# Optimization experiments

Hardware: AMD Instinct MI355X
Metric: run time of the kernel (lower is better)

The kernel has to match this reference:

```python
import jax, jax.numpy as jnp
import numpy as np

B, E, N, D, H = 4, 8, 1024, 1024, 4096


def setup_inputs() -> dict:
    key = jax.random.key(0)
    k1, k2, k3 = jax.random.split(key, 3)
    x = jax.random.normal(k1, (B, E, N, D), dtype=jnp.float32)
    # expert MLP weights: Linear(D,H) -> GELU -> Linear(H,D), per expert
    w1 = jax.random.normal(k2, (E, D, H), dtype=jnp.float32) * 0.02
    b1 = jnp.zeros((E, H), dtype=jnp.float32)
    w2 = jax.random.normal(k3, (E, H, D), dtype=jnp.float32) * 0.02
    b2 = jnp.zeros((E, D), dtype=jnp.float32)
    return {"x": x, "w1": w1, "b1": b1, "w2": w2, "b2": b2}


def reference(x, w1, b1, w2, b2):
    # x: [b, e, n, d]. Original rearranges to 'e b n d' and applies expert i
    # to slice i; a batched einsum over the expert axis is the same math.
    h = jnp.einsum('bend,edh->benh', x, w1) + b1[:, None, :]  # [b,e,n,H]
    h = jax.nn.gelu(h, approximate=False)  # torch nn.GELU default = exact erf
    out = jnp.einsum('benh,ehd->bend', h, w2) + b2[:, None, :]  # [b,e,n,d]
    return out
```

## Files before the change

### kernel.cpp

```cpp
#include <hip/hip_runtime.h>
#include <stdint.h>


typedef __attribute__((ext_vector_type(8))) short short8;
typedef __attribute__((ext_vector_type(4))) float f32x4;

__device__ __forceinline__ unsigned short f2b(float f){
  union { float f; unsigned int u; } v; v.f = f;
  unsigned int r = v.u + 0x7fffu + ((v.u >> 16) & 1u);
  return (unsigned short)(r >> 16);
}

__device__ __forceinline__ float gelu_fast(float v){
  float v2 = v * v;
  float w = v * (-2.302217529693f + -0.102943795894f * v2);
  float e = __builtin_amdgcn_exp2f(w);
  return v * __builtin_amdgcn_rcpf(1.0f + e);
}

__device__ __forceinline__ void glds16(const void* g, const void* l){
  __builtin_amdgcn_global_load_lds((const __attribute__((address_space(1))) uint32_t*)g,
                                   (__attribute__((address_space(3))) uint32_t*)l, 16, 0, 0);
}

#define BAR() do{ asm volatile("" ::: "memory"); __builtin_amdgcn_s_barrier(); asm volatile("" ::: "memory"); }while(0)


__global__ void cvt_x_kernel(const float* __restrict__ src, unsigned short* __restrict__ dst, int n4){
  int i = blockIdx.x * blockDim.x + threadIdx.x;
  int stride = gridDim.x * blockDim.x;
  for (; i < n4; i += stride){
    float4 v = ((const float4*)src)[i];
    ushort4 o;
    o.x = f2b(v.x); o.y = f2b(v.y); o.z = f2b(v.z); o.w = f2b(v.w);
    ((ushort4*)dst)[i] = o;
  }
}

__global__ void transpose_cvt(const float* __restrict__ src, unsigned short* __restrict__ dst, int R, int C){
  __shared__ float t[64][65];
  const int e = blockIdx.z;
  src += (size_t)e * R * C;
  dst += (size_t)e * R * C;
  const int r0 = blockIdx.y * 64, c0 = blockIdx.x * 64;
  const int tid = threadIdx.x;
  const int lr = tid >> 4;
  const int lc4 = (tid & 15) * 4;
  #pragma unroll
  for (int p2 = 0; p2 < 4; p2++){
    int r = lr + p2 * 16;
    float4 v = *(const float4*)(src + (size_t)(r0 + r) * C + (c0 + lc4));
    t[r][lc4+0] = v.x; t[r][lc4+1] = v.y; t[r][lc4+2] = v.z; t[r][lc4+3] = v.w;
  }
  __syncthreads();
  #pragma unroll
  for (int p2 = 0; p2 < 4; p2++){
    int c = lr + p2 * 16;
    ushort4 o;
    o.x = f2b(t[lc4+0][c]); o.y = f2b(t[lc4+1][c]);
    o.z = f2b(t[lc4+2][c]); o.w = f2b(t[lc4+3][c]);
    *(ushort4*)(dst + (size_t)(c0 + c) * R + (r0 + lc4)) = o;
  }
}


template<int PHASE1>
__global__ __launch_bounds__(512, 2) void gemm256(
    const unsigned short* __restrict__ A,
    const unsigned short* __restrict__ Bt,
    const float* __restrict__ bias,
    void* __restrict__ Out,
    int p0)
{
  constexpr int M  = 1024;
  constexpr int K  = PHASE1 ? 1024 : 4096;
  constexpr int Nd = PHASE1 ? 4096 : 1024;
  constexpr int TM = M / 256, TN = Nd / 256;
  constexpr int NT = K / 64;

  const int cpx = gridDim.x >> 3;
  const int bid = (blockIdx.x & 7) * cpx + (blockIdx.x >> 3);
  const int tn = bid % TN;
  const int t2 = bid / TN;
  const int tm = t2 % TM;
  const int cp = t2 / TM;
  const int p  = p0 + cp, e = p & 7;
  const int m0 = tm * 256, n0 = tn * 256;

  const unsigned short* Ag = A  + (size_t)(PHASE1 ? p : cp) * M * K + (size_t)m0 * K;
  const unsigned short* Bg = Bt + (size_t)e * Nd * K + (size_t)n0 * K;
  const float*          bp = bias + (size_t)e * Nd;

  __shared__ __align__(16) unsigned short lds[65536];

  const int tid = threadIdx.x;
  const int w = tid >> 6, lane = tid & 63;
  const int wr = w >> 2, wc = w & 3;
  const int c15 = lane & 15, q = lane >> 4;

  const int trow = (w << 3) + (lane >> 3);
  const int scol = ((lane & 7) ^ (trow & 7)) << 3;
  const unsigned short* pA0 = Ag + (size_t)(trow       ) * K + scol;
  const unsigned short* pA1 = Ag + (size_t)(trow +  64) * K + scol;
  const unsigned short* pA2 = Ag + (size_t)(trow + 128) * K + scol;
  const unsigned short* pA3 = Ag + (size_t)(trow + 192) * K + scol;
  const unsigned short* pB0 = Bg + (size_t)(trow       ) * K + scol;
  const unsigned short* pB1 = Bg + (size_t)(trow +  64) * K + scol;
  const unsigned short* pB2 = Bg + (size_t)(trow + 128) * K + scol;
  const unsigned short* pB3 = Bg + (size_t)(trow + 192) * K + scol;
  const int wof = w << 9;

  const int rA64 = (wr * 128 + c15) << 6;
  const int rB64 = (wc * 64  + c15) << 6;
  const int cx0 = ( q      ^ (c15 & 7)) << 3;
  const int cx1 = ((q ^ 4) ^ (c15 & 7)) << 3;

  float bv[4];
  #pragma unroll
  for (int nf = 0; nf < 4; ++nf) bv[nf] = bp[n0 + wc * 64 + nf * 16 + c15];

  f32x4 acc[8][4];
  #pragma unroll
  for (int i = 0; i < 8; i++)
    #pragma unroll
    for (int j = 0; j < 4; j++) acc[i][j] = (f32x4)(bv[j]);

  glds16(pA0, lds + wof);
  glds16(pA1, lds + wof + 4096);
  glds16(pA2, lds + wof + 8192);
  glds16(pA3, lds + wof + 12288);
  glds16(pB0, lds + wof + 32768);
  glds16(pB1, lds + wof + 32768 + 4096);
  glds16(pB2, lds + wof + 32768 + 8192);
  glds16(pB3, lds + wof + 32768 + 12288);
  glds16(pA0 + 64, lds + wof + 16384);
  glds16(pA1 + 64, lds + wof + 16384 + 4096);
  asm volatile("s_waitcnt vmcnt(2)" ::: "memory");
  BAR();

  short8 af[4][2], bf0[2][2], bf1[2][2];

#define TILE_BODY(CB, PF1, PF2, VM) do{                                         \
    constexpr int AB  = (CB) * 16384;                                           \
    constexpr int BB  = 32768 + (CB) * 16384;                                   \
    constexpr int ABn = ((CB) ^ 1) * 16384;                                     \
    constexpr int BBn = 32768 + (((CB) ^ 1) * 16384);                           \
    constexpr int O1  = (CB) ? 128 : 64;                                        \
    constexpr int O2  = (CB) ? 192 : 128;                                       \
       \
    _Pragma("unroll")                                                           \
    for (int mf = 0; mf < 4; ++mf){                                             \
      af[mf][0] = *(const short8*)(lds + AB + rA64 + mf * 1024 + cx0);          \
      af[mf][1] = *(const short8*)(lds + AB + rA64 + mf * 1024 + cx1);          \
    }                                                                           \
    _Pragma("unroll")                                                           \
    for (int nf = 0; nf < 2; ++nf){                                             \
      bf0[nf][0] = *(const short8*)(lds + BB + rB64 + nf * 1024 + cx0);         \
      bf0[nf][1] = *(const short8*)(lds + BB + rB64 + nf * 1024 + cx1);         \
    }                                                                           \
    if (PF1){ glds16(pA2 + O1, lds + ABn + 8192 + wof);                         \
              glds16(pA3 + O1, lds + ABn + 12288 + wof); }                      \
    BAR();                                                                      \
    __builtin_amdgcn_s_setprio(1);                                              \
    _Pragma("unroll")                                                           \
    for (int mf = 0; mf < 4; ++mf)                                              \
      _Pragma("unroll")                                                         \
      for (int nf = 0; nf < 2; ++nf){                                           \
        acc[mf][nf] = __builtin_amdgcn_mfma_f32_16x16x32_bf16(af[mf][0], bf0[nf][0], acc[mf][nf], 0, 0, 0); \
        acc[mf][nf] = __builtin_amdgcn_mfma_f32_16x16x32_bf16(af[mf][1], bf0[nf][1], acc[mf][nf], 0, 0, 0); \
      }                                                                         \
    __builtin_amdgcn_s_setprio(0);                                              \
    BAR();                                                                      \
                      \
    _Pragma("unroll")                                                           \
    for (int nf = 0; nf < 2; ++nf){                                             \
      bf1[nf][0] = *(const short8*)(lds + BB + rB64 + 2048 + nf * 1024 + cx0);  \
      bf1[nf][1] = *(const short8*)(lds + BB + rB64 + 2048 + nf * 1024 + cx1);  \
    }                                                                           \
    if (PF1){ glds16(pB0 + O1, lds + BBn + wof);                                \
              glds16(pB1 + O1, lds + BBn + 4096 + wof); }                       \
    BAR();                                                                      \
    __builtin_amdgcn_s_setprio(1);                                              \
    _Pragma("unroll")                                                           \
    for (int mf = 0; mf < 4; ++mf)                                              \
      _Pragma("unroll")                                                         \
      for (int nf = 0; nf < 2; ++nf){                                           \
        acc[mf][2+nf] = __builtin_amdgcn_mfma_f32_16x16x32_bf16(af[mf][0], bf1[nf][0], acc[mf][2+nf], 0, 0, 0); \
        acc[mf][2+nf] = __builtin_amdgcn_mfma_f32_16x16x32_bf16(af[mf][1], bf1[nf][1], acc[mf][2+nf], 0, 0, 0); \
      }                                                                         \
    __builtin_amdgcn_s_setprio(0);                                              \
    BAR();                                                                      \
                    \
    _Pragma("unroll")                                                           \
    for (int mf = 0; mf < 4; ++mf){                                             \
      af[mf][0] = *(const short8*)(lds + AB + rA64 + 4096 + mf * 1024 + cx0);   \
      af[mf][1] = *(const short8*)(lds + AB + rA64 + 4096 + mf * 1024 + cx1);   \
    }                                                                           \
    if (PF1){ glds16(pB2 + O1, lds + BBn + 8192 + wof);                         \
              glds16(pB3 + O1, lds + BBn + 12288 + wof); }                      \
    BAR();                                                                      \
    __builtin_amdgcn_s_setprio(1);                                              \
    _Pragma("unroll")                                                           \
    for (int mf = 0; mf < 4; ++mf)                                              \
      _Pragma("unroll")                                                         \
      for (int nf = 0; nf < 2; ++nf){                                           \
        acc[4+mf][2+nf] = __builtin_amdgcn_mfma_f32_16x16x32_bf16(af[mf][0], bf1[nf][0], acc[4+mf][2+nf], 0, 0, 0); \
        acc[4+mf][2+nf] = __builtin_amdgcn_mfma_f32_16x16x32_bf16(af[mf][1], bf1[nf][1], acc[4+mf][2+nf], 0, 0, 0); \
      }                                                                         \
    __builtin_amdgcn_s_setprio(0);                                              \
    BAR();                                                                      \
          \
    if (PF2){ glds16(pA0 + O2, lds + AB + wof);                                 \
              glds16(pA1 + O2, lds + AB + 4096 + wof); }                        \
    BAR();                                                                      \
    __builtin_amdgcn_s_setprio(1);                                              \
    _Pragma("unroll")                                                           \
    for (int mf = 0; mf < 4; ++mf)                                              \
      _Pragma("unroll")                                                         \
      for (int nf = 0; nf < 2; ++nf){                                           \
        acc[4+mf][nf] = __builtin_amdgcn_mfma_f32_16x16x32_bf16(af[mf][0], bf0[nf][0], acc[4+mf][nf], 0, 0, 0); \
        acc[4+mf][nf] = __builtin_amdgcn_mfma_f32_16x16x32_bf16(af[mf][1], bf0[nf][1], acc[4+mf][nf], 0, 0, 0); \
      }                                                                         \
    __builtin_amdgcn_s_setprio(0);                                              \
    if ((VM) >= 0){                                                             \
      if ((VM) == 2) asm volatile("s_waitcnt vmcnt(2)" ::: "memory");           \
      else           asm volatile("s_waitcnt vmcnt(0)" ::: "memory");           \
    }                                                                           \
    BAR();                                                                      \
  }while(0)

  for (int kt2 = 0; kt2 + 2 < NT; kt2 += 2){
    TILE_BODY(0, 1, 1, 2);
    TILE_BODY(1, 1, 1, 2);
    pA0 += 128; pA1 += 128; pA2 += 128; pA3 += 128;
    pB0 += 128; pB1 += 128; pB2 += 128; pB3 += 128;
  }
  TILE_BODY(0, 1, 0, 0);
  TILE_BODY(1, 0, 0, -1);
#undef TILE_BODY

  #pragma unroll
  for (int mf = 0; mf < 8; ++mf){
    const int row = m0 + wr * 128 + mf * 16 + q * 4;
    #pragma unroll
    for (int nf = 0; nf < 4; ++nf){
      const int col = n0 + wc * 64 + nf * 16 + c15;
      #pragma unroll
      for (int r = 0; r < 4; ++r){
        float v = acc[mf][nf][r];
        if constexpr (PHASE1){
          ((unsigned short*)Out)[(size_t)cp * M * Nd + (size_t)(row + r) * Nd + col] = f2b(gelu_fast(v));
        } else {
          ((float*)Out)[(size_t)p * M * Nd + (size_t)(row + r) * Nd + col] = v;
        }
      }
    }
  }
}


extern "C" void kernel_launch(void* const* d_in, const int* in_sizes, int n_in,
                              void* d_out, int out_size, void* d_ws, size_t ws_size,
                              hipStream_t stream){
  const float* x  = (const float*)d_in[0];
  const float* w1 = (const float*)d_in[1];
  const float* b1 = (const float*)d_in[2];
  const float* w2 = (const float*)d_in[3];
  const float* b2 = (const float*)d_in[4];
  float* out = (float*)d_out;

  unsigned short* xb  = (unsigned short*)d_ws;
  unsigned short* w1t = (unsigned short*)((char*)d_ws + ((size_t)64  << 20));
  unsigned short* w2t = (unsigned short*)((char*)d_ws + ((size_t)128 << 20));
  unsigned short* hb  = (unsigned short*)((char*)d_ws + ((size_t)192 << 20));

  size_t avail = ws_size > ((size_t)192 << 20) ? ws_size - ((size_t)192 << 20) : 0;
  int ppc = (int)(avail / ((size_t)8 << 20));
  if (ppc > 32) ppc = 32;
  if (ppc < 1) return;

  cvt_x_kernel<<<2048, 256, 0, stream>>>(x, xb, 8 * 1024 * 1024);
  transpose_cvt<<<dim3(64, 16, 8), 256, 0, stream>>>(w1, w1t, 1024, 4096);
  transpose_cvt<<<dim3(16, 64, 8), 256, 0, stream>>>(w2, w2t, 4096, 1024);

  for (int p0 = 0; p0 < 32; p0 += ppc){
    int np = (32 - p0 < ppc) ? (32 - p0) : ppc;
    gemm256<1><<<dim3(np * 4 * 16), 512, 0, stream>>>(xb, w1t, b1, hb, p0);
    gemm256<0><<<dim3(np * 4 * 4),  512, 0, stream>>>(hb, w2t, b2, out, p0);
  }
}
```

Before: 624.6 us.

## Restructure GEMM main loop to prefetch LDS fragments across phases with fewer barriers

Reworks the bf16 MFMA tile body so that A/B fragments for the next phase and next k-tile are read from LDS before the barrier that ends the current phase, cutting the number of barriers per tile from eight to four. It also reorders which global-to-LDS prefetches are issued in each phase (A rows 1 and 3 early, all four B slices together, A rows 0 and 2 late). The goal is to overlap LDS reads with MFMA work and reduce synchronization stalls. In exchange it holds more fragment registers live and depends on subtle ordering between LDS writes and reads across buffers, which could cause races or register pressure.

```diff
diff --git a/kernel.cpp b/kernel.cpp
--- a/kernel.cpp
+++ b/kernel.cpp
@@ -125,6 +125,26 @@
     #pragma unroll
     for (int j = 0; j < 4; j++) acc[i][j] = (f32x4)(bv[j]);
 
+  short8 afA[2][2], afB[2][2], bf0_[2][2], bf1_[2][2];
+
+#define LD(OFS) (*(const short8*)(lds + (OFS)))
+#define RD_AFA(BASE) do{ _Pragma("unroll") for (int mi=0;mi<2;++mi){ \
+    afA[mi][0] = LD((BASE) + rA64 + mi*1024 + cx0); \
+    afA[mi][1] = LD((BASE) + rA64 + mi*1024 + cx1); } }while(0)
+#define RD_AFB(BASE) do{ _Pragma("unroll") for (int mi=0;mi<2;++mi){ \
+    afB[mi][0] = LD((BASE) + rA64 + 2048 + mi*1024 + cx0); \
+    afB[mi][1] = LD((BASE) + rA64 + 2048 + mi*1024 + cx1); } }while(0)
+#define RD_BF0(BASE) do{ _Pragma("unroll") for (int nf=0;nf<2;++nf){ \
+    bf0_[nf][0] = LD((BASE) + rB64 + nf*1024 + cx0); \
+    bf0_[nf][1] = LD((BASE) + rB64 + nf*1024 + cx1); } }while(0)
+#define RD_BF1(BASE) do{ _Pragma("unroll") for (int nf=0;nf<2;++nf){ \
+    bf1_[nf][0] = LD((BASE) + rB64 + 2048 + nf*1024 + cx0); \
+    bf1_[nf][1] = LD((BASE) + rB64 + 2048 + nf*1024 + cx1); } }while(0)
+#define Q8(MO,NO,AF,BF) do{ _Pragma("unroll") for (int mi=0;mi<2;++mi) \
+    _Pragma("unroll") for (int nf=0;nf<2;++nf){ \
+      acc[(MO)+mi][(NO)+nf] = __builtin_amdgcn_mfma_f32_16x16x32_bf16(AF[mi][0], BF[nf][0], acc[(MO)+mi][(NO)+nf],0,0,0); \
+      acc[(MO)+mi][(NO)+nf] = __builtin_amdgcn_mfma_f32_16x16x32_bf16(AF[mi][1], BF[nf][1], acc[(MO)+mi][(NO)+nf],0,0,0); } }while(0)
+
   glds16(pA0, lds + wof);
   glds16(pA1, lds + wof + 4096);
   glds16(pA2, lds + wof + 8192);
@@ -134,110 +154,63 @@
   glds16(pB2, lds + wof + 32768 + 8192);
   glds16(pB3, lds + wof + 32768 + 12288);
   glds16(pA0 + 64, lds + wof + 16384);
-  glds16(pA1 + 64, lds + wof + 16384 + 4096);
+  glds16(pA2 + 64, lds + wof + 16384 + 8192);
   asm volatile("s_waitcnt vmcnt(2)" ::: "memory");
   BAR();
-
-  short8 af[4][2], bf0[2][2], bf1[2][2];
-
-#define TILE_BODY(CB, PF1, PF2, VM) do{                                         \
+  RD_AFA(0); RD_AFB(0); RD_BF0(32768);
+
+#define TILE_P(CB, PF1, PF2) do{                                                \
     constexpr int AB  = (CB) * 16384;                                           \
     constexpr int BB  = 32768 + (CB) * 16384;                                   \
     constexpr int ABn = ((CB) ^ 1) * 16384;                                     \
     constexpr int BBn = 32768 + (((CB) ^ 1) * 16384);                           \
     constexpr int O1  = (CB) ? 128 : 64;                                        \
     constexpr int O2  = (CB) ? 192 : 128;                                       \
-       \
-    _Pragma("unroll")                                                           \
-    for (int mf = 0; mf < 4; ++mf){                                             \
-      af[mf][0] = *(const short8*)(lds + AB + rA64 + mf * 1024 + cx0);          \
-      af[mf][1] = *(const short8*)(lds + AB + rA64 + mf * 1024 + cx1);          \
-    }                                                                           \
-    _Pragma("unroll")                                                           \
-    for (int nf = 0; nf < 2; ++nf){                                             \
-      bf0[nf][0] = *(const short8*)(lds + BB + rB64 + nf * 1024 + cx0);         \
-      bf0[nf][1] = *(const short8*)(lds + BB + rB64 + nf * 1024 + cx1);         \
-    }                                                                           \
-    if (PF1){ glds16(pA2 + O1, lds + ABn + 8192 + wof);                         \
+                        \
+    RD_BF1(BB);                                                                 \
+    if (PF1){ glds16(pA1 + O1, lds + ABn + 4096 + wof);                         \
               glds16(pA3 + O1, lds + ABn + 12288 + wof); }                      \
-    BAR();                                                                      \
-    __builtin_amdgcn_s_setprio(1);                                              \
-    _Pragma("unroll")                                                           \
-    for (int mf = 0; mf < 4; ++mf)                                              \
-      _Pragma("unroll")                                                         \
-      for (int nf = 0; nf < 2; ++nf){                                           \
-        acc[mf][nf] = __builtin_amdgcn_mfma_f32_16x16x32_bf16(af[mf][0], bf0[nf][0], acc[mf][nf], 0, 0, 0); \
-        acc[mf][nf] = __builtin_amdgcn_mfma_f32_16x16x32_bf16(af[mf][1], bf0[nf][1], acc[mf][nf], 0, 0, 0); \
-      }                                                                         \
-    __builtin_amdgcn_s_setprio(0);                                              \
-    BAR();                                                                      \
-                      \
-    _Pragma("unroll")                                                           \
-    for (int nf = 0; nf < 2; ++nf){                                             \
-      bf1[nf][0] = *(const short8*)(lds + BB + rB64 + 2048 + nf * 1024 + cx0);  \
-      bf1[nf][1] = *(const short8*)(lds + BB + rB64 + 2048 + nf * 1024 + cx1);  \
-    }                                                                           \
+    __builtin_amdgcn_s_setprio(1);                                              \
+    Q8(0,0,afA,bf0_); Q8(2,0,afB,bf0_);                                         \
+    __builtin_amdgcn_s_setprio(0);                                              \
+    BAR();                                                                      \
+        \
     if (PF1){ glds16(pB0 + O1, lds + BBn + wof);                                \
-              glds16(pB1 + O1, lds + BBn + 4096 + wof); }                       \
-    BAR();                                                                      \
-    __builtin_amdgcn_s_setprio(1);                                              \
-    _Pragma("unroll")                                                           \
-    for (int mf = 0; mf < 4; ++mf)                                              \
-      _Pragma("unroll")                                                         \
-      for (int nf = 0; nf < 2; ++nf){                                           \
-        acc[mf][2+nf] = __builtin_amdgcn_mfma_f32_16x16x32_bf16(af[mf][0], bf1[nf][0], acc[mf][2+nf], 0, 0, 0); \
-        acc[mf][2+nf] = __builtin_amdgcn_mfma_f32_16x16x32_bf16(af[mf][1], bf1[nf][1], acc[mf][2+nf], 0, 0, 0); \
-      }                                                                         \
-    __builtin_amdgcn_s_setprio(0);                                              \
-    BAR();                                                                      \
-                    \
-    _Pragma("unroll")                                                           \
-    for (int mf = 0; mf < 4; ++mf){                                             \
-      af[mf][0] = *(const short8*)(lds + AB + rA64 + 4096 + mf * 1024 + cx0);   \
-      af[mf][1] = *(const short8*)(lds + AB + rA64 + 4096 + mf * 1024 + cx1);   \
-    }                                                                           \
-    if (PF1){ glds16(pB2 + O1, lds + BBn + 8192 + wof);                         \
+              glds16(pB1 + O1, lds + BBn + 4096 + wof);                         \
+              glds16(pB2 + O1, lds + BBn + 8192 + wof);                         \
               glds16(pB3 + O1, lds + BBn + 12288 + wof); }                      \
-    BAR();                                                                      \
-    __builtin_amdgcn_s_setprio(1);                                              \
-    _Pragma("unroll")                                                           \
-    for (int mf = 0; mf < 4; ++mf)                                              \
-      _Pragma("unroll")                                                         \
-      for (int nf = 0; nf < 2; ++nf){                                           \
-        acc[4+mf][2+nf] = __builtin_amdgcn_mfma_f32_16x16x32_bf16(af[mf][0], bf1[nf][0], acc[4+mf][2+nf], 0, 0, 0); \
-        acc[4+mf][2+nf] = __builtin_amdgcn_mfma_f32_16x16x32_bf16(af[mf][1], bf1[nf][1], acc[4+mf][2+nf], 0, 0, 0); \
-      }                                                                         \
-    __builtin_amdgcn_s_setprio(0);                                              \
-    BAR();                                                                      \
-          \
+    __builtin_amdgcn_s_setprio(1);                                              \
+    Q8(0,2,afA,bf1_); Q8(2,2,afB,bf1_);                                         \
+    __builtin_amdgcn_s_setprio(0);                                              \
+    RD_AFA(AB + 4096);                                                          \
+    BAR();                                                                      \
+    \
+    RD_AFB(AB + 4096);                                                          \
     if (PF2){ glds16(pA0 + O2, lds + AB + wof);                                 \
-              glds16(pA1 + O2, lds + AB + 4096 + wof); }                        \
-    BAR();                                                                      \
-    __builtin_amdgcn_s_setprio(1);                                              \
-    _Pragma("unroll")                                                           \
-    for (int mf = 0; mf < 4; ++mf)                                              \
-      _Pragma("unroll")                                                         \
-      for (int nf = 0; nf < 2; ++nf){                                           \
-        acc[4+mf][nf] = __builtin_amdgcn_mfma_f32_16x16x32_bf16(af[mf][0], bf0[nf][0], acc[4+mf][nf], 0, 0, 0); \
-        acc[4+mf][nf] = __builtin_amdgcn_mfma_f32_16x16x32_bf16(af[mf][1], bf0[nf][1], acc[4+mf][nf], 0, 0, 0); \
-      }                                                                         \
-    __builtin_amdgcn_s_setprio(0);                                              \
-    if ((VM) >= 0){                                                             \
-      if ((VM) == 2) asm volatile("s_waitcnt vmcnt(2)" ::: "memory");           \
-      else           asm volatile("s_waitcnt vmcnt(0)" ::: "memory");           \
-    }                                                                           \
+              glds16(pA2 + O2, lds + AB + 8192 + wof); }                        \
+    __builtin_amdgcn_s_setprio(1);                                              \
+    Q8(4,2,afA,bf1_); Q8(6,2,afB,bf1_);                                         \
+    __builtin_amdgcn_s_setprio(0);                                              \
+    if (PF1){ if (PF2){ asm volatile("s_waitcnt vmcnt(2)" ::: "memory"); }      \
+              else    { asm volatile("s_waitcnt vmcnt(0)" ::: "memory"); } }    \
+    BAR();                                                                      \
+                \
+    __builtin_amdgcn_s_setprio(1);                                              \
+    Q8(4,0,afA,bf0_); Q8(6,0,afB,bf0_);                                         \
+    __builtin_amdgcn_s_setprio(0);                                              \
+    if (PF1){ RD_AFA(ABn); RD_AFB(ABn); RD_BF0(BBn); }                          \
     BAR();                                                                      \
   }while(0)
 
-  for (int kt2 = 0; kt2 + 2 < NT; kt2 += 2){
-    TILE_BODY(0, 1, 1, 2);
-    TILE_BODY(1, 1, 1, 2);
+  for (int kt2 = 0; kt2 < NT - 2; kt2 += 2){
+    TILE_P(0, 1, 1);
+    TILE_P(1, 1, 1);
     pA0 += 128; pA1 += 128; pA2 += 128; pA3 += 128;
     pB0 += 128; pB1 += 128; pB2 += 128; pB3 += 128;
   }
-  TILE_BODY(0, 1, 0, 0);
-  TILE_BODY(1, 0, 0, -1);
-#undef TILE_BODY
+  TILE_P(0, 1, 0);
+  TILE_P(1, 0, 0);
+#undef TILE_P
 
   #pragma unroll
   for (int mf = 0; mf < 8; ++mf){
```

Result: slower. 780.9 us (+25.0%).

## Reorder prefetch issue and split waitcnts to load A rows just in time

Applied to the files above, without the earlier changes.

Changes the order of the global-to-LDS prefetches inside the double-buffered GEMM tile loop. B is now prefetched first, and the A sub-tiles are grouped so the half that the next tile reads first arrives earliest. A second, finer vmcnt wait is added mid-tile, letting more loads stay in flight while only the data needed next must have landed. This aims to hide more global latency behind MFMA work, at the cost of depending on correct ordering and vmcnt accounting.

```diff
diff --git a/kernel.cpp b/kernel.cpp
--- a/kernel.cpp
+++ b/kernel.cpp
@@ -24,6 +24,10 @@
 }
 
 #define BAR() do{ asm volatile("" ::: "memory"); __builtin_amdgcn_s_barrier(); asm volatile("" ::: "memory"); }while(0)
+#define VMW(N) do{ if ((N)==6) asm volatile("s_waitcnt vmcnt(6)":::"memory"); \
+  else if ((N)==4) asm volatile("s_waitcnt vmcnt(4)":::"memory"); \
+  else if ((N)==2) asm volatile("s_waitcnt vmcnt(2)":::"memory"); \
+  else if ((N)==0) asm volatile("s_waitcnt vmcnt(0)":::"memory"); }while(0)
 
 
 __global__ void cvt_x_kernel(const float* __restrict__ src, unsigned short* __restrict__ dst, int n4){
@@ -134,20 +138,20 @@
   glds16(pB2, lds + wof + 32768 + 8192);
   glds16(pB3, lds + wof + 32768 + 12288);
   glds16(pA0 + 64, lds + wof + 16384);
-  glds16(pA1 + 64, lds + wof + 16384 + 4096);
+  glds16(pA2 + 64, lds + wof + 16384 + 8192);
   asm volatile("s_waitcnt vmcnt(2)" ::: "memory");
   BAR();
 
   short8 af[4][2], bf0[2][2], bf1[2][2];
 
-#define TILE_BODY(CB, PF1, PF2, VM) do{                                         \
+#define TILE_BODY(CB, SB1, SA2, W1, W3) do{                                     \
     constexpr int AB  = (CB) * 16384;                                           \
     constexpr int BB  = 32768 + (CB) * 16384;                                   \
     constexpr int ABn = ((CB) ^ 1) * 16384;                                     \
     constexpr int BBn = 32768 + (((CB) ^ 1) * 16384);                           \
     constexpr int O1  = (CB) ? 128 : 64;                                        \
     constexpr int O2  = (CB) ? 192 : 128;                                       \
-       \
+              \
     _Pragma("unroll")                                                           \
     for (int mf = 0; mf < 4; ++mf){                                             \
       af[mf][0] = *(const short8*)(lds + AB + rA64 + mf * 1024 + cx0);          \
@@ -158,8 +162,8 @@
       bf0[nf][0] = *(const short8*)(lds + BB + rB64 + nf * 1024 + cx0);         \
       bf0[nf][1] = *(const short8*)(lds + BB + rB64 + nf * 1024 + cx1);         \
     }                                                                           \
-    if (PF1){ glds16(pA2 + O1, lds + ABn + 8192 + wof);                         \
-              glds16(pA3 + O1, lds + ABn + 12288 + wof); }                      \
+    if (SB1){ glds16(pB0 + O1, lds + BBn + wof);                                \
+              glds16(pB1 + O1, lds + BBn + 4096 + wof); }                       \
     BAR();                                                                      \
     __builtin_amdgcn_s_setprio(1);                                              \
     _Pragma("unroll")                                                           \
@@ -171,14 +175,14 @@
       }                                                                         \
     __builtin_amdgcn_s_setprio(0);                                              \
     BAR();                                                                      \
-                      \
+                  \
     _Pragma("unroll")                                                           \
     for (int nf = 0; nf < 2; ++nf){                                             \
       bf1[nf][0] = *(const short8*)(lds + BB + rB64 + 2048 + nf * 1024 + cx0);  \
       bf1[nf][1] = *(const short8*)(lds + BB + rB64 + 2048 + nf * 1024 + cx1);  \
     }                                                                           \
-    if (PF1){ glds16(pB0 + O1, lds + BBn + wof);                                \
-              glds16(pB1 + O1, lds + BBn + 4096 + wof); }                       \
+    if (SB1){ glds16(pB2 + O1, lds + BBn + 8192 + wof);                         \
+              glds16(pB3 + O1, lds + BBn + 12288 + wof); }                      \
     BAR();                                                                      \
     __builtin_amdgcn_s_setprio(1);                                              \
     _Pragma("unroll")                                                           \
@@ -189,15 +193,16 @@
         acc[mf][2+nf] = __builtin_amdgcn_mfma_f32_16x16x32_bf16(af[mf][1], bf1[nf][1], acc[mf][2+nf], 0, 0, 0); \
       }                                                                         \
     __builtin_amdgcn_s_setprio(0);                                              \
-    BAR();                                                                      \
-                    \
+    if ((W1) >= 0) VMW(W1);                                                     \
+    BAR();                                                                      \
+                           \
     _Pragma("unroll")                                                           \
     for (int mf = 0; mf < 4; ++mf){                                             \
       af[mf][0] = *(const short8*)(lds + AB + rA64 + 4096 + mf * 1024 + cx0);   \
       af[mf][1] = *(const short8*)(lds + AB + rA64 + 4096 + mf * 1024 + cx1);   \
     }                                                                           \
-    if (PF1){ glds16(pB2 + O1, lds + BBn + 8192 + wof);                         \
-              glds16(pB3 + O1, lds + BBn + 12288 + wof); }                      \
+    if (SB1){ glds16(pA1 + O1, lds + ABn + 4096 + wof);                         \
+              glds16(pA3 + O1, lds + ABn + 12288 + wof); }                      \
     BAR();                                                                      \
     __builtin_amdgcn_s_setprio(1);                                              \
     _Pragma("unroll")                                                           \
@@ -210,8 +215,8 @@
     __builtin_amdgcn_s_setprio(0);                                              \
     BAR();                                                                      \
           \
-    if (PF2){ glds16(pA0 + O2, lds + AB + wof);                                 \
-              glds16(pA1 + O2, lds + AB + 4096 + wof); }                        \
+    if (SA2){ glds16(pA0 + O2, lds + AB + wof);                                 \
+              glds16(pA2 + O2, lds + AB + 8192 + wof); }                        \
     BAR();                                                                      \
     __builtin_amdgcn_s_setprio(1);                                              \
     _Pragma("unroll")                                                           \
@@ -222,21 +227,18 @@
         acc[4+mf][nf] = __builtin_amdgcn_mfma_f32_16x16x32_bf16(af[mf][1], bf0[nf][1], acc[4+mf][nf], 0, 0, 0); \
       }                                                                         \
     __builtin_amdgcn_s_setprio(0);                                              \
-    if ((VM) >= 0){                                                             \
-      if ((VM) == 2) asm volatile("s_waitcnt vmcnt(2)" ::: "memory");           \
-      else           asm volatile("s_waitcnt vmcnt(0)" ::: "memory");           \
-    }                                                                           \
+    if ((W3) >= 0) VMW(W3);                                                     \
     BAR();                                                                      \
   }while(0)
 
-  for (int kt2 = 0; kt2 + 2 < NT; kt2 += 2){
-    TILE_BODY(0, 1, 1, 2);
-    TILE_BODY(1, 1, 1, 2);
+  for (int kt2 = 0; kt2 < NT - 2; kt2 += 2){
+    TILE_BODY(0, 1, 1, 6, 4);
+    TILE_BODY(1, 1, 1, 6, 4);
     pA0 += 128; pA1 += 128; pA2 += 128; pA3 += 128;
     pB0 += 128; pB1 += 128; pB2 += 128; pB3 += 128;
   }
-  TILE_BODY(0, 1, 0, 0);
-  TILE_BODY(1, 0, 0, -1);
+  TILE_BODY(0, 1, 0, 6, 2);
+  TILE_BODY(1, 0, 0, 0, -1);
 #undef TILE_BODY
 
   #pragma unroll
```

Result: faster. 610.8 us (-2.2%).
